# Optimization experiments

Hardware: AMD Instinct MI355X
Metric: run time of the kernel (lower is better)

The kernel has to match this reference:

```python
import jax, jax.numpy as jnp
import numpy as np


def setup_inputs() -> dict:
    key = jax.random.key(0)
    ks = jax.random.split(key, 7)
    B, C, W, H = 4, 128, 64, 64
    Cq = C // 8
    x = jax.random.normal(ks[0], (B, C, W, H), jnp.float32)
    wq = jax.random.normal(ks[1], (Cq, C), jnp.float32) * 0.05
    bq = jax.random.normal(ks[2], (Cq,), jnp.float32) * 0.05
    wk = jax.random.normal(ks[3], (Cq, C), jnp.float32) * 0.05
    bk = jax.random.normal(ks[4], (Cq,), jnp.float32) * 0.05
    wv = jax.random.normal(ks[5], (C, C), jnp.float32) * 0.05
    bv = jax.random.normal(ks[6], (C,), jnp.float32) * 0.05
    gamma = jnp.ones((1,), jnp.float32)
    return {"x": x, "wq": wq, "bq": bq, "wk": wk, "bk": bk,
            "wv": wv, "bv": bv, "gamma": gamma}


def reference(x, wq, bq, wk, bk, wv, bv, gamma):
    B, C, W, H = x.shape
    N = W * H
    xf = x.reshape(B, C, N)  # flatten spatial dims (W fastest over H, as torch .view)
    # 1x1 convs == per-position linear maps
    q = jnp.einsum('dc,bcn->bnd', wq, xf) + bq            # [B, N, C//8]
    k = jnp.einsum('dc,bcn->bdn', wk, xf) + bk[:, None]   # [B, C//8, N]
    v = jnp.einsum('dc,bcn->bdn', wv, xf) + bv[:, None]   # [B, C, N]
    energy = jnp.einsum('bnd,bdm->bnm', q, k)             # [B, N, N]
    # block-causal mask: position i may attend only to j < (i//W + 1)*W
    i = jnp.arange(N)
    j = jnp.arange(N)
    masked = j[None, :] >= ((i[:, None] // W) + 1) * W    # True -> -inf
    energy = jnp.where(masked[None, :, :], -jnp.inf, energy)
    attention = jax.nn.softmax(energy, axis=-1)           # [B, N, N]
    # out[b,c,n] = sum_m V[b,c,m] * attn[b,n,m]  (torch bmm(V, attn^T))
    out = jnp.einsum('bcm,bnm->bcn', v, attention).reshape(B, C, W, H)
    out = gamma * out + x
    return (out, attention)
```

## Files before the change

kernel.cpp:

```cpp
#include <hip/hip_runtime.h>
#include <hip/hip_bf16.h>


typedef __attribute__((ext_vector_type(8))) short short8;
typedef __attribute__((ext_vector_type(16))) float float16;
typedef __attribute__((ext_vector_type(4))) float floatx4;

__device__ __forceinline__ ushort f2bf(float f) {
  union { float f; uint u; } v; v.f = f;
  return (ushort)((v.u + 0x7FFFu + ((v.u >> 16) & 1u)) >> 16);
}

#define LDS_BARRIER()                                             \
  do {                                                            \
    __builtin_amdgcn_sched_barrier(0);                            \
    asm volatile("s_waitcnt lgkmcnt(0)" ::: "memory");            \
    __builtin_amdgcn_sched_barrier(0);                            \
    __builtin_amdgcn_s_barrier();                                 \
    __builtin_amdgcn_sched_barrier(0);                            \
  } while (0)

__global__ __launch_bounds__(512, 2) void qkv_kernel(
    const float* __restrict__ x,
    const float* __restrict__ wq, const float* __restrict__ bq,
    const float* __restrict__ wk, const float* __restrict__ bk,
    const float* __restrict__ wv, const float* __restrict__ bv,
    ushort* __restrict__ qT, ushort* __restrict__ kT, ushort* __restrict__ vo) {
  __shared__ float xs[128 * 64];
  const int nt = blockIdx.x, b = blockIdx.y;
  const int n0 = nt * 64;
  const float* xb = x + (size_t)b * 524288 + n0;
  for (int idx = threadIdx.x; idx < 8192; idx += 512) {
    int c = idx >> 6, n = idx & 63;
    xs[idx] = xb[(size_t)c * 4096 + n];
  }
  __syncthreads();
  const int n = threadIdx.x & 63;
  const int og = __builtin_amdgcn_readfirstlane((int)(threadIdx.x >> 6));
  float acc[20];
#pragma unroll
  for (int i = 0; i < 20; i++) {
    int o = og + 8 * i;
    acc[i] = (i < 2) ? bq[o] : (i < 4) ? bk[o - 16] : bv[o - 32];
  }
#pragma unroll 4
  for (int c = 0; c < 128; c++) {
    float xr = xs[c * 64 + n];
#pragma unroll
    for (int i = 0; i < 20; i++) {
      int o = og + 8 * i;
      const float* wr = (i < 2) ? (wq + o * 128)
                      : (i < 4) ? (wk + (o - 16) * 128)
                                : (wv + (o - 32) * 128);
      acc[i] += wr[c] * xr;
    }
  }
  const size_t pos = (size_t)b * 4096 + n0 + n;
#pragma unroll
  for (int i = 0; i < 20; i++) {
    int o = og + 8 * i;
    if (i < 2)      qT[pos * 16 + o]      = f2bf(acc[i]);
    else if (i < 4) kT[pos * 16 + o - 16] = f2bf(acc[i]);
    else vo[(size_t)b * 524288 + (size_t)(o - 32) * 4096 + n0 + n] = f2bf(acc[i]);
  }
}

__global__ __launch_bounds__(512, 4) void fused_attn_kernel(
    const ushort* __restrict__ qT, const ushort* __restrict__ kT,
    const ushort* __restrict__ vws, const float* __restrict__ x,
    const float* __restrict__ g,
    float* __restrict__ attn, float* __restrict__ out) {
  __shared__ __align__(16) ushort Pt[8][32 * 72];
  __shared__ __align__(16) float red[32][8];
  const int bx = blockIdx.x;
  const int b = bx & 3;
  const int v_ = bx >> 2;
  const int half = v_ & 1;
  const int u = v_ >> 1;
  const int rb = (u < 32) ? u : 95 - u;
  const int S = rb + 1;
  const int lane = threadIdx.x & 63;
  const int w = __builtin_amdgcn_readfirstlane((int)(threadIdx.x >> 6));
  const int q = w & 3;
  const int hh = w >> 2;
  const int nblk = rb * 64 + half * 32;
  const int l31 = lane & 31;
  const int h = lane >> 5;
  const int hk = h * 8;
  const ushort* qb = qT + (size_t)b * 65536;
  const ushort* kb = kT + (size_t)b * 65536;
  const ushort* vp = vws + (size_t)b * 524288;
  float* ab = attn + (size_t)b * 16777216;

  const short8 qa = *(const short8*)(qb + (size_t)(nblk + l31) * 16 + hk);

  float16 zero16;
#pragma unroll
  for (int i = 0; i < 16; i++) zero16[i] = 0.f;

  float sume[16];
#pragma unroll
  for (int i = 0; i < 16; i++) sume[i] = 0.f;
  for (int s = w; s < S; s += 8) {
    const int m0 = s * 64;
#pragma unroll
    for (int mh = 0; mh < 2; mh++) {
      short8 kf = *(const short8*)(kb + (size_t)(m0 + mh * 32 + l31) * 16 + hk);
      float16 e = __builtin_amdgcn_mfma_f32_32x32x16_bf16(qa, kf, zero16, 0, 0, 0);
#pragma unroll
      for (int r = 0; r < 16; r++) sume[r] += __expf(e[r]);
    }
  }
#pragma unroll
  for (int r = 0; r < 16; r++) {
#pragma unroll
    for (int off = 1; off <= 16; off <<= 1)
      sume[r] += __shfl_xor(sume[r], off, 64);
  }
  if (l31 == 0) {
#pragma unroll
    for (int r = 0; r < 16; r++) {
      int row = (r & 3) + 8 * (r >> 2) + 4 * h;
      red[row][w] = sume[r];
    }
  }
  __syncthreads();
  float inv[16];
#pragma unroll
  for (int r = 0; r < 16; r++) {
    int row = (r & 3) + 8 * (r >> 2) + 4 * h;
    const float* pr = &red[row][0];
    float t = ((pr[0] + pr[1]) + (pr[2] + pr[3])) +
              ((pr[4] + pr[5]) + (pr[6] + pr[7]));
    inv[r] = 1.0f / t;
  }

  float16 acc = zero16;
  for (int s0 = 0; s0 < S; s0 += 8) {
    const int sl = (S - s0 < 8) ? (S - s0) : 8;
    if (w < sl) {
      const int m0 = (s0 + w) * 64;
      ushort* Pb = &Pt[w][0];
#pragma unroll
      for (int mh = 0; mh < 2; mh++) {
        short8 kf = *(const short8*)(kb + (size_t)(m0 + mh * 32 + l31) * 16 + hk);
        float16 e = __builtin_amdgcn_mfma_f32_32x32x16_bf16(qa, kf, zero16, 0, 0, 0);
#pragma unroll
        for (int r = 0; r < 16; r++) {
          int row = (r & 3) + 8 * (r >> 2) + 4 * h;
          float p = __expf(e[r]) * inv[r];
          ab[(size_t)(nblk + row) * 4096 + m0 + mh * 32 + l31] = p;
          Pb[row * 72 + mh * 32 + l31] = f2bf(p);
        }
      }
    }
    LDS_BARRIER();
    for (int ss = hh; ss < sl; ss += 2) {
      const int m0 = (s0 + ss) * 64;
      const ushort* vrow = vp + (size_t)(q * 32 + l31) * 4096 + m0 + hk;
      const ushort* Pr = &Pt[ss][l31 * 72 + hk];
#pragma unroll
      for (int kk = 0; kk < 4; kk++) {
        short8 a  = *(const short8*)(vrow + kk * 16);
        short8 bf = *(const short8*)(Pr + kk * 16);
        acc = __builtin_amdgcn_mfma_f32_32x32x16_bf16(a, bf, acc, 0, 0, 0);
      }
    }
    LDS_BARRIER();
  }

  float* accx = (float*)&Pt[0][0];
  if (hh == 1) {
#pragma unroll
    for (int reg = 0; reg < 16; reg++)
      accx[reg * 256 + q * 64 + lane] = acc[reg];
  }
  __syncthreads();
  if (hh == 0) {
#pragma unroll
    for (int reg = 0; reg < 16; reg++)
      acc[reg] += accx[reg * 256 + q * 64 + lane];
  }

  const int M = S * 64;
  const int Z4 = (4096 - M) >> 2;
  const floatx4 z = {0.f, 0.f, 0.f, 0.f};
#pragma unroll
  for (int r = 0; r < 4; r++) {
    floatx4* dst = (floatx4*)(ab + (size_t)(nblk + w * 4 + r) * 4096 + M);
    for (int i4 = lane; i4 < Z4; i4 += 64) dst[i4] = z;
  }

  if (hh == 0) {
    const float gamma = g[0];
#pragma unroll
    for (int reg = 0; reg < 16; reg++) {
      int row = (reg & 3) + 8 * (reg >> 2) + 4 * h;
      int c = q * 32 + row;
      int n = nblk + l31;
      size_t off = (size_t)b * 524288 + (size_t)c * 4096 + n;
      out[off] = gamma * acc[reg] + x[off];
    }
  }
}

extern "C" void kernel_launch(void* const* d_in, const int* in_sizes, int n_in,
                              void* d_out, int out_size, void* d_ws, size_t ws_size,
                              hipStream_t stream) {
  const float* x  = (const float*)d_in[0];
  const float* wq = (const float*)d_in[1];
  const float* bq = (const float*)d_in[2];
  const float* wk = (const float*)d_in[3];
  const float* bk = (const float*)d_in[4];
  const float* wv = (const float*)d_in[5];
  const float* bv = (const float*)d_in[6];
  const float* gm = (const float*)d_in[7];
  float* out  = (float*)d_out;
  float* attn = out + 2097152;
  ushort* qTw = (ushort*)d_ws;
  ushort* kTw = qTw + 262144;
  ushort* vws = qTw + 524288;

  qkv_kernel<<<dim3(64, 4), 512, 0, stream>>>(x, wq, bq, wk, bk, wv, bv, qTw, kTw, vws);
  fused_attn_kernel<<<dim3(512), 512, 0, stream>>>(qTw, kTw, vws, x, gm, attn, out);
}
```

Baseline: 347.5 us.

## Split attention kernel waves into compute and store roles via LDS staging

Waves 0-3 now compute the probability tiles and run the PV MFMAs, while waves 4-7 copy fp32 probabilities staged in LDS out to the attention matrix using 16-byte vectorized stores. The store waves also handle the zero-fill of the masked region. This replaces strided scalar global stores with coalesced float4 stores and lets the attention writeback overlap with the PV matmul. In exchange only half the waves do math, the per-iteration chunk shrinks from 8 to 4 tiles (more barriers), and extra LDS is used for the fp32 staging buffer, which may lower occupancy.

```diff
diff --git a/kernel.cpp b/kernel.cpp
--- a/kernel.cpp
+++ b/kernel.cpp
@@ -70,7 +70,8 @@
     const ushort* __restrict__ vws, const float* __restrict__ x,
     const float* __restrict__ g,
     float* __restrict__ attn, float* __restrict__ out) {
-  __shared__ __align__(16) ushort Pt[8][32 * 72];
+  __shared__ __align__(16) ushort Pt[4][32 * 72];
+  __shared__ __align__(16) float Pf[4][32 * 64];
   __shared__ __align__(16) float red[32][8];
   const int bx = blockIdx.x;
   const int b = bx & 3;
@@ -81,8 +82,8 @@
   const int S = rb + 1;
   const int lane = threadIdx.x & 63;
   const int w = __builtin_amdgcn_readfirstlane((int)(threadIdx.x >> 6));
+  const int role = w >> 2;
   const int q = w & 3;
-  const int hh = w >> 2;
   const int nblk = rb * 64 + half * 32;
   const int l31 = lane & 31;
   const int h = lane >> 5;
@@ -136,11 +137,12 @@
   }
 
   float16 acc = zero16;
-  for (int s0 = 0; s0 < S; s0 += 8) {
-    const int sl = (S - s0 < 8) ? (S - s0) : 8;
-    if (w < sl) {
-      const int m0 = (s0 + w) * 64;
-      ushort* Pb = &Pt[w][0];
+  for (int s0 = 0; s0 < S; s0 += 4) {
+    const int sl = (S - s0 < 4) ? (S - s0) : 4;
+    if (role == 0 && q < sl) {
+      const int m0 = (s0 + q) * 64;
+      ushort* Pb = &Pt[q][0];
+      float* Pc = &Pf[q][0];
 #pragma unroll
       for (int mh = 0; mh < 2; mh++) {
         short8 kf = *(const short8*)(kb + (size_t)(m0 + mh * 32 + l31) * 16 + hk);
@@ -149,49 +151,50 @@
         for (int r = 0; r < 16; r++) {
           int row = (r & 3) + 8 * (r >> 2) + 4 * h;
           float p = __expf(e[r]) * inv[r];
-          ab[(size_t)(nblk + row) * 4096 + m0 + mh * 32 + l31] = p;
+          Pc[row * 64 + mh * 32 + l31] = p;
           Pb[row * 72 + mh * 32 + l31] = f2bf(p);
         }
       }
     }
     LDS_BARRIER();
-    for (int ss = hh; ss < sl; ss += 2) {
-      const int m0 = (s0 + ss) * 64;
-      const ushort* vrow = vp + (size_t)(q * 32 + l31) * 4096 + m0 + hk;
-      const ushort* Pr = &Pt[ss][l31 * 72 + hk];
-#pragma unroll
-      for (int kk = 0; kk < 4; kk++) {
-        short8 a  = *(const short8*)(vrow + kk * 16);
-        short8 bf = *(const short8*)(Pr + kk * 16);
-        acc = __builtin_amdgcn_mfma_f32_32x32x16_bf16(a, bf, acc, 0, 0, 0);
+
+    if (role == 1 && q < sl) {
+      const int m0 = (s0 + q) * 64;
+      const int r4 = lane >> 4;
+      const int c4 = (lane & 15) * 4;
+#pragma unroll
+      for (int i = 0; i < 8; i++) {
+        int row = i * 4 + r4;
+        floatx4 val = *(const floatx4*)&Pf[q][row * 64 + c4];
+        *(floatx4*)(ab + (size_t)(nblk + row) * 4096 + m0 + c4) = val;
       }
     }
+    if (role == 0) {
+      for (int ss = 0; ss < sl; ss++) {
+        const int m0 = (s0 + ss) * 64;
+        const ushort* vrow = vp + (size_t)(q * 32 + l31) * 4096 + m0 + hk;
+        const ushort* Pr = &Pt[ss][l31 * 72 + hk];
+#pragma unroll
+        for (int kk = 0; kk < 4; kk++) {
+          short8 a  = *(const short8*)(vrow + kk * 16);
+          short8 bf = *(const short8*)(Pr + kk * 16);
+          acc = __builtin_amdgcn_mfma_f32_32x32x16_bf16(a, bf, acc, 0, 0, 0);
+        }
+      }
+    }
     LDS_BARRIER();
   }
 
-  float* accx = (float*)&Pt[0][0];
-  if (hh == 1) {
-#pragma unroll
-    for (int reg = 0; reg < 16; reg++)
-      accx[reg * 256 + q * 64 + lane] = acc[reg];
-  }
-  __syncthreads();
-  if (hh == 0) {
-#pragma unroll
-    for (int reg = 0; reg < 16; reg++)
-      acc[reg] += accx[reg * 256 + q * 64 + lane];
-  }
-
-  const int M = S * 64;
-  const int Z4 = (4096 - M) >> 2;
-  const floatx4 z = {0.f, 0.f, 0.f, 0.f};
-#pragma unroll
-  for (int r = 0; r < 4; r++) {
-    floatx4* dst = (floatx4*)(ab + (size_t)(nblk + w * 4 + r) * 4096 + M);
-    for (int i4 = lane; i4 < Z4; i4 += 64) dst[i4] = z;
-  }
-
-  if (hh == 0) {
+  if (role == 1) {
+    const int M = S * 64;
+    const int Z4 = (4096 - M) >> 2;
+    const floatx4 z = {0.f, 0.f, 0.f, 0.f};
+#pragma unroll
+    for (int r = 0; r < 8; r++) {
+      floatx4* dst = (floatx4*)(ab + (size_t)(nblk + q * 8 + r) * 4096 + M);
+      for (int i4 = lane; i4 < Z4; i4 += 64) dst[i4] = z;
+    }
+  } else {
     const float gamma = g[0];
 #pragma unroll
     for (int reg = 0; reg < 16; reg++) {
```

After: 365.7 us. +5.2%, slower.
